# Kernel optimization log

Hardware: AMD Instinct MI355X
Metric: run time of the kernel (lower is better)

The kernel has to match this reference:

```python
import jax, jax.numpy as jnp
import numpy as np
import math

FACTOR = 5


def _prob_attention(queries, keys, values, index_sample):
    # queries/keys/values: [B, H, L, D]; index_sample: [L_Q, sample_k] int
    B, H, L_Q, D = queries.shape
    L_K = keys.shape[2]
    u = min(FACTOR * int(math.ceil(math.log(L_Q))), L_Q)  # n_top queries

    # --- _prob_QK: random-sampled scores, heuristic M, top-u query selection ---
    # gather sampled keys per query position: [B, H, L_Q, sample_k, D]
    K_sample = keys[:, :, index_sample, :]
    Q_K_sample = jnp.einsum('bhqd,bhqkd->bhqk', queries, K_sample)  # [B,H,L_Q,sample_k]
    M = Q_K_sample.max(axis=-1) - Q_K_sample.sum(axis=-1) / L_K      # [B,H,L_Q]
    M_top = jax.lax.top_k(M, u)[1]                                   # [B,H,u] indices

    # gather the selected queries and compute full scores against all keys
    Q_reduce = jnp.take_along_axis(queries, M_top[..., None], axis=2)  # [B,H,u,D]
    scores = jnp.einsum('bhud,bhkd->bhuk', Q_reduce, keys)             # [B,H,u,L_K]

    # scale: original does `scale = self.scale or 1/sqrt(D)`; with scale=True this
    # multiplies by True (i.e. *1), so scores are left unscaled -- faithful.

    # --- causal ProbMask: triu(1) rows gathered at the selected query indices ---
    causal = jnp.triu(jnp.ones((L_Q, L_K), dtype=bool), 1)  # [L_Q, L_K]
    row_mask = causal[M_top]                                 # [B,H,u,L_K]
    scores = jnp.where(row_mask, -jnp.inf, scores)

    attn = jax.nn.softmax(scores, axis=-1)                   # [B,H,u,L_K]

    # --- initial context (mask_flag=True): cumulative sum of V over time ---
    context = jnp.cumsum(values, axis=2)                     # [B,H,L_Q,D]

    # --- scatter-update context at selected query positions ---
    upd = jnp.einsum('bhuk,bhkd->bhud', attn, values)        # [B,H,u,D]
    b_idx = jnp.arange(B)[:, None, None]
    h_idx = jnp.arange(H)[None, :, None]
    context = context.at[b_idx, h_idx, M_top].set(upd)

    return jnp.transpose(context, (0, 2, 1, 3))              # [B,L_Q,H,D]


def setup_inputs() -> dict:
    key = jax.random.key(0)
    kq, kk, kv, ki = jax.random.split(key, 4)
    B, H, L, D = 4, 8, 2048, 64
    sample_k = FACTOR * int(math.ceil(math.log(L)))  # 40
    queries = jax.random.normal(kq, (B, H, L, D), dtype=jnp.float32)
    keys = jax.random.normal(kk, (B, H, L, D), dtype=jnp.float32)
    values = jax.random.normal(kv, (B, H, L, D), dtype=jnp.float32)
    index_sample = jax.random.randint(ki, (L, sample_k), 0, L)
    return {"queries": queries, "keys": keys, "values": values,
            "index_sample": index_sample}


def reference(queries, keys, values, index_sample):
    return _prob_attention(queries, keys, values, index_sample)
```

## Files before the change

### kernel.cpp

```cpp
#include <hip/hip_runtime.h>
#include <math.h>

#define B_ 4
#define H_ 8
#define L_ 2048
#define D_ 64
#define SK_ 40
#define U_ 40
#define NSEG 32
#define SEGLEN 64
#define CK 256
#define NCHUNK (L_ / CK)
#define QG 8
#define NQG (U_ / QG)

__global__ __launch_bounds__(1024) void k_compute_M(
    const float* __restrict__ Q, const float* __restrict__ K,
    const int* __restrict__ idxs, float* __restrict__ M) {
  int blk = blockIdx.x;
  int x = blk & 7;
  int j = blk >> 3;
  int bh = ((j >> 7) << 3) | x;
  int qc = j & 127;
  int wave = threadIdx.x >> 6;
  int lane = threadIdx.x & 63;
  int q = qc * 16 + wave;

  int g  = lane >> 3;
  int li = lane & 7;

  const float4* qrow = (const float4*)(Q + ((size_t)bh * L_ + q) * D_);
  float4 qa = qrow[li], qb = qrow[li + 8];
  int myidx = (lane < SK_) ? idxs[q * SK_ + lane] : 0;
  const float* Kb = K + (size_t)bh * L_ * D_;

  int kis[5];
#pragma unroll
  for (int t = 0; t < 5; ++t) kis[t] = __shfl(myidx, t * 8 + g, 64);
  float4 ka[5], kb[5];
#pragma unroll
  for (int t = 0; t < 5; ++t) {
    const float4* kr = (const float4*)(Kb + (size_t)kis[t] * D_);
    ka[t] = kr[li];
    kb[t] = kr[li + 8];
  }

  float d[5];
#pragma unroll
  for (int t = 0; t < 5; ++t) {
    d[t] = qa.x * ka[t].x + qa.y * ka[t].y + qa.z * ka[t].z + qa.w * ka[t].w
         + qb.x * kb[t].x + qb.y * kb[t].y + qb.z * kb[t].z + qb.w * kb[t].w;
  }
  float mx = -INFINITY, sm = 0.f;
#pragma unroll
  for (int t = 0; t < 5; ++t) {
    float v = d[t];
    v += __shfl_xor(v, 1, 64);
    v += __shfl_xor(v, 2, 64);
    v += __shfl_xor(v, 4, 64);
    mx = fmaxf(mx, v);
    sm += v;
  }
  mx = fmaxf(mx, __shfl_xor(mx, 8, 64));
  mx = fmaxf(mx, __shfl_xor(mx, 16, 64));
  mx = fmaxf(mx, __shfl_xor(mx, 32, 64));
  sm += __shfl_xor(sm, 8, 64);
  sm += __shfl_xor(sm, 16, 64);
  sm += __shfl_xor(sm, 32, 64);
  if (lane == 0) M[bh * L_ + q] = mx - sm * (1.0f / (float)L_);
}

__global__ __launch_bounds__(1024) void k_topk(
    const float* __restrict__ M, int* __restrict__ Mtop) {
  __shared__ unsigned keys[L_];
  __shared__ int hist[256];
  __shared__ int Gs[256];
  __shared__ unsigned ctl_prefix;
  __shared__ int ctl_need, ctl_cnt, ctl_min;
  __shared__ int wmin[16];
  int bh = blockIdx.x;
  int tid = threadIdx.x;

  for (int i = tid; i < L_; i += 1024) {
    unsigned u = __float_as_uint(M[bh * L_ + i]);
    keys[i] = (u & 0x80000000u) ? ~u : (u | 0x80000000u);
  }
  if (tid == 0) { ctl_prefix = 0u; ctl_need = U_; ctl_cnt = 0; }
  __syncthreads();

  unsigned prefix = 0u, pmask = 0u;
#pragma unroll
  for (int pass = 0; pass < 4; ++pass) {
    int shift = 24 - 8 * pass;
    if (tid < 256) hist[tid] = 0;
    __syncthreads();
    for (int i = tid; i < L_; i += 1024) {
      unsigned k = keys[i];
      if ((k & pmask) == prefix) atomicAdd(&hist[(k >> shift) & 0xffu], 1);
    }
    __syncthreads();
    if (tid < 64) {
      int b0 = tid * 4;
      int h0 = hist[b0], h1 = hist[b0 + 1], h2 = hist[b0 + 2], h3 = hist[b0 + 3];
      int gs = h0 + h1 + h2 + h3;
      int S = gs;
#pragma unroll
      for (int d = 1; d < 64; d <<= 1) {
        int v = __shfl_down(S, d, 64);
        if (tid + d < 64) S += v;
      }
      int E = S - gs;
      Gs[b0 + 3] = E;
      Gs[b0 + 2] = E + h3;
      Gs[b0 + 1] = E + h3 + h2;
      Gs[b0 + 0] = E + h3 + h2 + h1;
    }
    __syncthreads();
    int need = ctl_need;
    if (tid < 256) {
      int G = Gs[tid], h = hist[tid];
      if (G < need && need <= G + h) {
        ctl_prefix = prefix | ((unsigned)tid << shift);
        ctl_need = need - G;
      }
    }
    __syncthreads();
    prefix = ctl_prefix;
    pmask |= (0xffu << shift);
  }

  unsigned v40 = prefix;
  int tiesNeeded = ctl_need;
  __syncthreads();

  for (int i = tid; i < L_; i += 1024) {
    if (keys[i] > v40) {
      int slot = atomicAdd(&ctl_cnt, 1);
      Mtop[bh * U_ + slot] = i;
    }
  }
  __syncthreads();
  int base = ctl_cnt;
  int last = -1;
  for (int t = 0; t < tiesNeeded; ++t) {
    int lmin = 0x7fffffff;
    for (int i = tid; i < L_; i += 1024)
      if (keys[i] == v40 && i > last) lmin = min(lmin, i);
#pragma unroll
    for (int d = 32; d > 0; d >>= 1) lmin = min(lmin, __shfl_xor(lmin, d, 64));
    if ((tid & 63) == 0) wmin[tid >> 6] = lmin;
    __syncthreads();
    if (tid == 0) {
      int m = wmin[0];
      for (int w = 1; w < 16; ++w) m = min(m, wmin[w]);
      Mtop[bh * U_ + base + t] = m;
      ctl_min = m;
    }
    __syncthreads();
    last = ctl_min;
  }
}

__global__ __launch_bounds__(256) void k_segsum(
    const float* __restrict__ V, float* __restrict__ segsum) {
  int gw = (blockIdx.x * blockDim.x + threadIdx.x) >> 6;
  int lane = threadIdx.x & 63;
  int seg = gw & (NSEG - 1);
  int bh  = gw >> 5;
  const float* Vb = V + ((size_t)bh * L_ + seg * SEGLEN) * D_;
  float s = 0.f;
#pragma unroll 8
  for (int l = 0; l < SEGLEN; ++l) s += Vb[(size_t)l * D_ + lane];
  segsum[((size_t)bh * NSEG + seg) * D_ + lane] = s;
}

__global__ __launch_bounds__(256) void k_cumsum(
    const float* __restrict__ V, const float* __restrict__ segsum,
    float* __restrict__ out) {
  int gw = (blockIdx.x * blockDim.x + threadIdx.x) >> 6;
  int lane = threadIdx.x & 63;
  int seg = gw & (NSEG - 1);
  int bh  = gw >> 5;
  int b = bh >> 3, h = bh & 7;
  float off = 0.f;
  for (int s = 0; s < seg; ++s)
    off += segsum[((size_t)bh * NSEG + s) * D_ + lane];
  const float* Vb = V + ((size_t)bh * L_ + seg * SEGLEN) * D_;
  float run = off;
  for (int l = 0; l < SEGLEN; ++l) {
    run += Vb[(size_t)l * D_ + lane];
    int gl = seg * SEGLEN + l;
    out[(((size_t)b * L_ + gl) * H_ + h) * D_ + lane] = run;
  }
}

__global__ __launch_bounds__(256) void k_attn_part(
    const float* __restrict__ Q, const float* __restrict__ K,
    const float* __restrict__ V, const int* __restrict__ Mtop,
    float* __restrict__ pm, float* __restrict__ ps, float* __restrict__ pacc) {
  int blk = blockIdx.x;
  int x = blk & 7;
  int j = blk >> 3;
  int bh = (j / 40) * 8 + x;
  int rem = j % 40;
  int c  = rem / NQG;
  int qg = rem % NQG;

  int tid = threadIdx.x;
  int w = tid >> 6, lane = tid & 63;
  __shared__ float Qs[QG][D_];
  __shared__ float P[QG][CK];
  __shared__ float pvred[4][QG][D_];
  __shared__ int q0s[QG];
  if (tid < QG) q0s[tid] = Mtop[bh * U_ + qg * QG + tid];
  __syncthreads();
  for (int i = tid; i < QG * D_; i += 256) {
    int u = i >> 6, d = i & 63;
    Qs[u][d] = Q[((size_t)bh * L_ + q0s[u]) * D_ + d];
  }
  __syncthreads();

  int kg = c * CK + tid;
  const float4* kr = (const float4*)(K + ((size_t)bh * L_ + kg) * D_);
  float4 kv[16];
#pragma unroll
  for (int j4 = 0; j4 < 16; ++j4) kv[j4] = kr[j4];
#pragma unroll
  for (int u = 0; u < QG; ++u) {
    float acc = 0.f;
#pragma unroll
    for (int j4 = 0; j4 < 16; ++j4) {
      float4 qv = *(const float4*)&Qs[u][j4 * 4];
      acc += qv.x * kv[j4].x + qv.y * kv[j4].y + qv.z * kv[j4].z + qv.w * kv[j4].w;
    }
    P[u][tid] = (kg <= q0s[u]) ? acc : -INFINITY;
  }
  __syncthreads();

#pragma unroll
  for (int uu = 0; uu < 2; ++uu) {
    int u = w * 2 + uu;
    float v0 = P[u][lane], v1 = P[u][lane + 64];
    float v2 = P[u][lane + 128], v3 = P[u][lane + 192];
    float m = fmaxf(fmaxf(v0, v1), fmaxf(v2, v3));
    for (int o = 32; o > 0; o >>= 1) m = fmaxf(m, __shfl_xor(m, o, 64));
    float e0 = (v0 == -INFINITY) ? 0.f : expf(v0 - m);
    float e1 = (v1 == -INFINITY) ? 0.f : expf(v1 - m);
    float e2 = (v2 == -INFINITY) ? 0.f : expf(v2 - m);
    float e3 = (v3 == -INFINITY) ? 0.f : expf(v3 - m);
    float s = e0 + e1 + e2 + e3;
    for (int o = 32; o > 0; o >>= 1) s += __shfl_xor(s, o, 64);
    P[u][lane] = e0; P[u][lane + 64] = e1;
    P[u][lane + 128] = e2; P[u][lane + 192] = e3;
    if (lane == 0) {
      int p = (bh * NCHUNK + c) * U_ + qg * QG + u;
      pm[p] = m; ps[p] = s;
    }
  }
  __syncthreads();

  const float* Vb = V + ((size_t)bh * L_ + c * CK + w * 64) * D_;
  float acc[QG];
#pragma unroll
  for (int u = 0; u < QG; ++u) acc[u] = 0.f;
  for (int k4 = 0; k4 < 16; ++k4) {
    float4 pv[QG];
#pragma unroll
    for (int u = 0; u < QG; ++u) pv[u] = *(const float4*)&P[u][w * 64 + k4 * 4];
    float va = Vb[(size_t)(k4 * 4 + 0) * D_ + lane];
    float vb = Vb[(size_t)(k4 * 4 + 1) * D_ + lane];
    float vc = Vb[(size_t)(k4 * 4 + 2) * D_ + lane];
    float vd = Vb[(size_t)(k4 * 4 + 3) * D_ + lane];
#pragma unroll
    for (int u = 0; u < QG; ++u)
      acc[u] += pv[u].x * va + pv[u].y * vb + pv[u].z * vc + pv[u].w * vd;
  }
#pragma unroll
  for (int u = 0; u < QG; ++u) pvred[w][u][lane] = acc[u];
  __syncthreads();
#pragma unroll
  for (int uu = 0; uu < 2; ++uu) {
    int u = w * 2 + uu;
    float tot = pvred[0][u][lane] + pvred[1][u][lane] +
                pvred[2][u][lane] + pvred[3][u][lane];
    int p = (bh * NCHUNK + c) * U_ + qg * QG + u;
    pacc[(size_t)p * 64 + lane] = tot;
  }
}

__global__ __launch_bounds__(256) void k_attn_reduce(
    const float* __restrict__ pm, const float* __restrict__ ps,
    const float* __restrict__ pacc, const int* __restrict__ Mtop,
    float* __restrict__ out) {
  int g = blockIdx.x * 4 + (threadIdx.x >> 6);
  int lane = threadIdx.x & 63;
  int bh = g / U_, u = g % U_;
  int b = bh >> 3, h = bh & 7;
  int q0 = Mtop[bh * U_ + u];
  float pmv[NCHUNK];
  float M = -INFINITY;
#pragma unroll
  for (int c = 0; c < NCHUNK; ++c) {
    pmv[c] = pm[(bh * NCHUNK + c) * U_ + u];
    M = fmaxf(M, pmv[c]);
  }
  float T = 0.f, o = 0.f;
#pragma unroll
  for (int c = 0; c < NCHUNK; ++c) {
    float wgt = (pmv[c] == -INFINITY) ? 0.f : expf(pmv[c] - M);
    T += ps[(bh * NCHUNK + c) * U_ + u] * wgt;
    o += pacc[((size_t)(bh * NCHUNK + c) * U_ + u) * 64 + lane] * wgt;
  }
  out[(((size_t)b * L_ + q0) * H_ + h) * D_ + lane] = o / T;
}

extern "C" void kernel_launch(void* const* d_in, const int* in_sizes, int n_in,
                              void* d_out, int out_size, void* d_ws, size_t ws_size,
                              hipStream_t stream) {
  const float* Q = (const float*)d_in[0];
  const float* K = (const float*)d_in[1];
  const float* V = (const float*)d_in[2];
  const int* idxs = (const int*)d_in[3];
  float* out = (float*)d_out;

  char* ws = (char*)d_ws;
  float* M      = (float*)(ws + 0);
  float* segsum = (float*)(ws + 262144);
  int*   Mtop   = (int*)(ws + 524288);
  float* pm     = (float*)(ws + 532480);
  float* ps     = (float*)(ws + 573440);
  float* pacc   = (float*)(ws + 614400);

  k_compute_M<<<(B_ * H_ * L_) / 16, 1024, 0, stream>>>(Q, K, idxs, M);
  k_topk<<<B_ * H_, 1024, 0, stream>>>(M, Mtop);
  k_segsum<<<(B_ * H_ * NSEG) / 4, 256, 0, stream>>>(V, segsum);
  k_cumsum<<<(B_ * H_ * NSEG) / 4, 256, 0, stream>>>(V, segsum, out);
  k_attn_part<<<B_ * H_ * NCHUNK * NQG, 256, 0, stream>>>(Q, K, V, Mtop, pm, ps, pacc);
  k_attn_reduce<<<(B_ * H_ * U_) / 4, 256, 0, stream>>>(pm, ps, pacc, Mtop, out);
}
```

Before: 84.29 us.

## Fuse chunked attention and reduction into single kernel with online softmax

Replaces the split-K attention partial kernel and separate reduction kernel with one kernel where each block iterates over all key chunks, keeping running max/sum and rescaling accumulators (online softmax). This removes a launch and the workspace round-trip for partial max, sum and accumulators. In exchange the grid shrinks by the chunk count, so each block does serial work over the full key length with lower parallelism.

After: 142.9 us. 69.5% more time.

```diff
diff --git a/kernel.cpp b/kernel.cpp
--- a/kernel.cpp
+++ b/kernel.cpp
@@ -37,6 +37,7 @@
   int kis[5];
 #pragma unroll
   for (int t = 0; t < 5; ++t) kis[t] = __shfl(myidx, t * 8 + g, 64);
+
   float4 ka[5], kb[5];
 #pragma unroll
   for (int t = 0; t < 5; ++t) {
@@ -194,23 +195,25 @@
   }
 }
 
-__global__ __launch_bounds__(256) void k_attn_part(
+__global__ __launch_bounds__(256) void k_attn(
     const float* __restrict__ Q, const float* __restrict__ K,
     const float* __restrict__ V, const int* __restrict__ Mtop,
-    float* __restrict__ pm, float* __restrict__ ps, float* __restrict__ pacc) {
+    float* __restrict__ out) {
   int blk = blockIdx.x;
   int x = blk & 7;
   int j = blk >> 3;
-  int bh = (j / 40) * 8 + x;
-  int rem = j % 40;
-  int c  = rem / NQG;
-  int qg = rem % NQG;
+  int bh = (j / NQG) * 8 + x;
+  int qg = j % NQG;
+  int b = bh >> 3, h = bh & 7;
 
   int tid = threadIdx.x;
   int w = tid >> 6, lane = tid & 63;
   __shared__ float Qs[QG][D_];
   __shared__ float P[QG][CK];
   __shared__ float pvred[4][QG][D_];
+  __shared__ float scaleO[QG];
+  __shared__ float pfac[QG];
+  __shared__ float sfin[QG];
   __shared__ int q0s[QG];
   if (tid < QG) q0s[tid] = Mtop[bh * U_ + qg * QG + tid];
   __syncthreads();
@@ -218,100 +221,94 @@
     int u = i >> 6, d = i & 63;
     Qs[u][d] = Q[((size_t)bh * L_ + q0s[u]) * D_ + d];
   }
-  __syncthreads();
-
-  int kg = c * CK + tid;
-  const float4* kr = (const float4*)(K + ((size_t)bh * L_ + kg) * D_);
-  float4 kv[16];
-#pragma unroll
-  for (int j4 = 0; j4 < 16; ++j4) kv[j4] = kr[j4];
-#pragma unroll
-  for (int u = 0; u < QG; ++u) {
-    float acc = 0.f;
-#pragma unroll
-    for (int j4 = 0; j4 < 16; ++j4) {
-      float4 qv = *(const float4*)&Qs[u][j4 * 4];
-      acc += qv.x * kv[j4].x + qv.y * kv[j4].y + qv.z * kv[j4].z + qv.w * kv[j4].w;
-    }
-    P[u][tid] = (kg <= q0s[u]) ? acc : -INFINITY;
-  }
-  __syncthreads();
-
-#pragma unroll
-  for (int uu = 0; uu < 2; ++uu) {
-    int u = w * 2 + uu;
-    float v0 = P[u][lane], v1 = P[u][lane + 64];
-    float v2 = P[u][lane + 128], v3 = P[u][lane + 192];
-    float m = fmaxf(fmaxf(v0, v1), fmaxf(v2, v3));
-    for (int o = 32; o > 0; o >>= 1) m = fmaxf(m, __shfl_xor(m, o, 64));
-    float e0 = (v0 == -INFINITY) ? 0.f : expf(v0 - m);
-    float e1 = (v1 == -INFINITY) ? 0.f : expf(v1 - m);
-    float e2 = (v2 == -INFINITY) ? 0.f : expf(v2 - m);
-    float e3 = (v3 == -INFINITY) ? 0.f : expf(v3 - m);
-    float s = e0 + e1 + e2 + e3;
-    for (int o = 32; o > 0; o >>= 1) s += __shfl_xor(s, o, 64);
-    P[u][lane] = e0; P[u][lane + 64] = e1;
-    P[u][lane + 128] = e2; P[u][lane + 192] = e3;
-    if (lane == 0) {
-      int p = (bh * NCHUNK + c) * U_ + qg * QG + u;
-      pm[p] = m; ps[p] = s;
-    }
-  }
-  __syncthreads();
-
-  const float* Vb = V + ((size_t)bh * L_ + c * CK + w * 64) * D_;
+
+  float m_run[2] = {-INFINITY, -INFINITY};
+  float s_run[2] = {0.f, 0.f};
   float acc[QG];
 #pragma unroll
   for (int u = 0; u < QG; ++u) acc[u] = 0.f;
-  for (int k4 = 0; k4 < 16; ++k4) {
-    float4 pv[QG];
-#pragma unroll
-    for (int u = 0; u < QG; ++u) pv[u] = *(const float4*)&P[u][w * 64 + k4 * 4];
-    float va = Vb[(size_t)(k4 * 4 + 0) * D_ + lane];
-    float vb = Vb[(size_t)(k4 * 4 + 1) * D_ + lane];
-    float vc = Vb[(size_t)(k4 * 4 + 2) * D_ + lane];
-    float vd = Vb[(size_t)(k4 * 4 + 3) * D_ + lane];
+  __syncthreads();
+
+  for (int c = 0; c < NCHUNK; ++c) {
+    int kg = c * CK + tid;
+    const float4* kr = (const float4*)(K + ((size_t)bh * L_ + kg) * D_);
+    float4 kv[16];
+#pragma unroll
+    for (int j4 = 0; j4 < 16; ++j4) kv[j4] = kr[j4];
+#pragma unroll
+    for (int u = 0; u < QG; ++u) {
+      float a = 0.f;
+#pragma unroll
+      for (int j4 = 0; j4 < 16; ++j4) {
+        float4 qv = *(const float4*)&Qs[u][j4 * 4];
+        a += qv.x * kv[j4].x + qv.y * kv[j4].y + qv.z * kv[j4].z + qv.w * kv[j4].w;
+      }
+      P[u][tid] = (kg <= q0s[u]) ? a : -INFINITY;
+    }
+    __syncthreads();
+
+#pragma unroll
+    for (int uu = 0; uu < 2; ++uu) {
+      int u = w * 2 + uu;
+      float v0 = P[u][lane], v1 = P[u][lane + 64];
+      float v2 = P[u][lane + 128], v3 = P[u][lane + 192];
+      float m = fmaxf(fmaxf(v0, v1), fmaxf(v2, v3));
+      for (int o = 32; o > 0; o >>= 1) m = fmaxf(m, __shfl_xor(m, o, 64));
+      float e0 = (v0 == -INFINITY) ? 0.f : expf(v0 - m);
+      float e1 = (v1 == -INFINITY) ? 0.f : expf(v1 - m);
+      float e2 = (v2 == -INFINITY) ? 0.f : expf(v2 - m);
+      float e3 = (v3 == -INFINITY) ? 0.f : expf(v3 - m);
+      float s = e0 + e1 + e2 + e3;
+      for (int o = 32; o > 0; o >>= 1) s += __shfl_xor(s, o, 64);
+      P[u][lane] = e0; P[u][lane + 64] = e1;
+      P[u][lane + 128] = e2; P[u][lane + 192] = e3;
+      float so, pf;
+      if (m == -INFINITY) {
+        so = 1.f; pf = 0.f;
+      } else {
+        float mnew = fmaxf(m_run[uu], m);
+        so = (m_run[uu] == -INFINITY) ? 0.f : expf(m_run[uu] - mnew);
+        pf = expf(m - mnew);
+        m_run[uu] = mnew;
+      }
+      s_run[uu] = s_run[uu] * so + s * pf;
+      if (lane == 0) { scaleO[u] = so; pfac[u] = pf; }
+    }
+    __syncthreads();
+
+    const float* Vb = V + ((size_t)bh * L_ + c * CK + w * 64) * D_;
+    float pv[QG];
+#pragma unroll
+    for (int u = 0; u < QG; ++u) pv[u] = 0.f;
+    for (int k4 = 0; k4 < 16; ++k4) {
+      float4 pw[QG];
+#pragma unroll
+      for (int u = 0; u < QG; ++u) pw[u] = *(const float4*)&P[u][w * 64 + k4 * 4];
+      float va = Vb[(size_t)(k4 * 4 + 0) * D_ + lane];
+      float vb = Vb[(size_t)(k4 * 4 + 1) * D_ + lane];
+      float vc = Vb[(size_t)(k4 * 4 + 2) * D_ + lane];
+      float vd = Vb[(size_t)(k4 * 4 + 3) * D_ + lane];
+#pragma unroll
+      for (int u = 0; u < QG; ++u)
+        pv[u] += pw[u].x * va + pw[u].y * vb + pw[u].z * vc + pw[u].w * vd;
+    }
 #pragma unroll
     for (int u = 0; u < QG; ++u)
-      acc[u] += pv[u].x * va + pv[u].y * vb + pv[u].z * vc + pv[u].w * vd;
-  }
+      acc[u] = acc[u] * scaleO[u] + pv[u] * pfac[u];
+    __syncthreads();
+  }
+
 #pragma unroll
   for (int u = 0; u < QG; ++u) pvred[w][u][lane] = acc[u];
+  if (lane == 0) { sfin[w * 2] = s_run[0]; sfin[w * 2 + 1] = s_run[1]; }
   __syncthreads();
 #pragma unroll
   for (int uu = 0; uu < 2; ++uu) {
     int u = w * 2 + uu;
     float tot = pvred[0][u][lane] + pvred[1][u][lane] +
                 pvred[2][u][lane] + pvred[3][u][lane];
-    int p = (bh * NCHUNK + c) * U_ + qg * QG + u;
-    pacc[(size_t)p * 64 + lane] = tot;
-  }
-}
-
-__global__ __launch_bounds__(256) void k_attn_reduce(
-    const float* __restrict__ pm, const float* __restrict__ ps,
-    const float* __restrict__ pacc, const int* __restrict__ Mtop,
-    float* __restrict__ out) {
-  int g = blockIdx.x * 4 + (threadIdx.x >> 6);
-  int lane = threadIdx.x & 63;
-  int bh = g / U_, u = g % U_;
-  int b = bh >> 3, h = bh & 7;
-  int q0 = Mtop[bh * U_ + u];
-  float pmv[NCHUNK];
-  float M = -INFINITY;
-#pragma unroll
-  for (int c = 0; c < NCHUNK; ++c) {
-    pmv[c] = pm[(bh * NCHUNK + c) * U_ + u];
-    M = fmaxf(M, pmv[c]);
-  }
-  float T = 0.f, o = 0.f;
-#pragma unroll
-  for (int c = 0; c < NCHUNK; ++c) {
-    float wgt = (pmv[c] == -INFINITY) ? 0.f : expf(pmv[c] - M);
-    T += ps[(bh * NCHUNK + c) * U_ + u] * wgt;
-    o += pacc[((size_t)(bh * NCHUNK + c) * U_ + u) * 64 + lane] * wgt;
-  }
-  out[(((size_t)b * L_ + q0) * H_ + h) * D_ + lane] = o / T;
+    out[(((size_t)b * L_ + q0s[u]) * H_ + h) * D_ + lane] = tot / sfin[u];
+  }
 }
 
 extern "C" void kernel_launch(void* const* d_in, const int* in_sizes, int n_in,
@@ -327,14 +324,10 @@
   float* M      = (float*)(ws + 0);
   float* segsum = (float*)(ws + 262144);
   int*   Mtop   = (int*)(ws + 524288);
-  float* pm     = (float*)(ws + 532480);
-  float* ps     = (float*)(ws + 573440);
-  float* pacc   = (float*)(ws + 614400);
 
   k_compute_M<<<(B_ * H_ * L_) / 16, 1024, 0, stream>>>(Q, K, idxs, M);
   k_topk<<<B_ * H_, 1024, 0, stream>>>(M, Mtop);
   k_segsum<<<(B_ * H_ * NSEG) / 4, 256, 0, stream>>>(V, segsum);
   k_cumsum<<<(B_ * H_ * NSEG) / 4, 256, 0, stream>>>(V, segsum, out);
-  k_attn_part<<<B_ * H_ * NCHUNK * NQG, 256, 0, stream>>>(Q, K, V, Mtop, pm, ps, pacc);
-  k_attn_reduce<<<(B_ * H_ * U_) / 4, 256, 0, stream>>>(pm, ps, pacc, Mtop, out);
-}
+  k_attn<<<B_ * H_ * NQG, 256, 0, stream>>>(Q, K, V, Mtop, out);
+}
```

## Fuse cumsum of V into the M-computation kernel as extra blocks

Applied to the files above, without the earlier changes.

Replaces the separate segment-sum and cumulative-sum kernels with 32 extra 1024-thread blocks prepended to the M-computation launch. Each extra block handles one (b,h) pair, computing 16 segment totals in shared memory and then writing the prefix sums. This removes two kernel launches and the segsum workspace round-trip, letting the cumsum overlap with the sampled-QK work. The trade-off is that each cumsum block is long-running and serial (128 rows per thread, two passes over V), and may become a tail on the fused launch.

New measurement: 69.18 us. -17.9%, faster.

```diff
diff --git a/kernel.cpp b/kernel.cpp
--- a/kernel.cpp
+++ b/kernel.cpp
@@ -7,17 +7,39 @@
 #define D_ 64
 #define SK_ 40
 #define U_ 40
-#define NSEG 32
-#define SEGLEN 64
 #define CK 256
 #define NCHUNK (L_ / CK)
 #define QG 8
 #define NQG (U_ / QG)
-
-__global__ __launch_bounds__(1024) void k_compute_M(
+#define CSB 32
+
+__global__ __launch_bounds__(1024) void k_mcs(
     const float* __restrict__ Q, const float* __restrict__ K,
-    const int* __restrict__ idxs, float* __restrict__ M) {
-  int blk = blockIdx.x;
+    const int* __restrict__ idxs, const float* __restrict__ V,
+    float* __restrict__ M, float* __restrict__ out) {
+  if (blockIdx.x < CSB) {
+    __shared__ float segtot[16][64];
+    int bh = blockIdx.x;
+    int b = bh >> 3, h = bh & 7;
+    int t = threadIdx.x;
+    int seg = t >> 6, d = t & 63;
+    const float* Vb = V + (size_t)bh * L_ * D_;
+    int base = seg * 128;
+    float s = 0.f;
+    for (int l = 0; l < 128; ++l) s += Vb[(size_t)(base + l) * D_ + d];
+    segtot[seg][d] = s;
+    __syncthreads();
+    float run = 0.f;
+    for (int ss = 0; ss < seg; ++ss) run += segtot[ss][d];
+    for (int l = 0; l < 128; ++l) {
+      int gl = base + l;
+      run += Vb[(size_t)gl * D_ + d];
+      out[(((size_t)b * L_ + gl) * H_ + h) * D_ + d] = run;
+    }
+    return;
+  }
+
+  int blk = blockIdx.x - CSB;
   int x = blk & 7;
   int j = blk >> 3;
   int bh = ((j >> 7) << 3) | x;
@@ -37,6 +59,7 @@
   int kis[5];
 #pragma unroll
   for (int t = 0; t < 5; ++t) kis[t] = __shfl(myidx, t * 8 + g, 64);
+
   float4 ka[5], kb[5];
 #pragma unroll
   for (int t = 0; t < 5; ++t) {
@@ -158,39 +181,6 @@
     }
     __syncthreads();
     last = ctl_min;
-  }
-}
-
-__global__ __launch_bounds__(256) void k_segsum(
-    const float* __restrict__ V, float* __restrict__ segsum) {
-  int gw = (blockIdx.x * blockDim.x + threadIdx.x) >> 6;
-  int lane = threadIdx.x & 63;
-  int seg = gw & (NSEG - 1);
-  int bh  = gw >> 5;
-  const float* Vb = V + ((size_t)bh * L_ + seg * SEGLEN) * D_;
-  float s = 0.f;
-#pragma unroll 8
-  for (int l = 0; l < SEGLEN; ++l) s += Vb[(size_t)l * D_ + lane];
-  segsum[((size_t)bh * NSEG + seg) * D_ + lane] = s;
-}
-
-__global__ __launch_bounds__(256) void k_cumsum(
-    const float* __restrict__ V, const float* __restrict__ segsum,
-    float* __restrict__ out) {
-  int gw = (blockIdx.x * blockDim.x + threadIdx.x) >> 6;
-  int lane = threadIdx.x & 63;
-  int seg = gw & (NSEG - 1);
-  int bh  = gw >> 5;
-  int b = bh >> 3, h = bh & 7;
-  float off = 0.f;
-  for (int s = 0; s < seg; ++s)
-    off += segsum[((size_t)bh * NSEG + s) * D_ + lane];
-  const float* Vb = V + ((size_t)bh * L_ + seg * SEGLEN) * D_;
-  float run = off;
-  for (int l = 0; l < SEGLEN; ++l) {
-    run += Vb[(size_t)l * D_ + lane];
-    int gl = seg * SEGLEN + l;
-    out[(((size_t)b * L_ + gl) * H_ + h) * D_ + lane] = run;
   }
 }
 
@@ -325,16 +315,13 @@
 
   char* ws = (char*)d_ws;
   float* M      = (float*)(ws + 0);
-  float* segsum = (float*)(ws + 262144);
-  int*   Mtop   = (int*)(ws + 524288);
-  float* pm     = (float*)(ws + 532480);
-  float* ps     = (float*)(ws + 573440);
-  float* pacc   = (float*)(ws + 614400);
-
-  k_compute_M<<<(B_ * H_ * L_) / 16, 1024, 0, stream>>>(Q, K, idxs, M);
+  int*   Mtop   = (int*)(ws + 262144);
+  float* pm     = (float*)(ws + 270336);
+  float* ps     = (float*)(ws + 311296);
+  float* pacc   = (float*)(ws + 352256);
+
+  k_mcs<<<CSB + (B_ * H_ * L_) / 16, 1024, 0, stream>>>(Q, K, idxs, V, M, out);
   k_topk<<<B_ * H_, 1024, 0, stream>>>(M, Mtop);
-  k_segsum<<<(B_ * H_ * NSEG) / 4, 256, 0, stream>>>(V, segsum);
-  k_cumsum<<<(B_ * H_ * NSEG) / 4, 256, 0, stream>>>(V, segsum, out);
   k_attn_part<<<B_ * H_ * NCHUNK * NQG, 256, 0, stream>>>(Q, K, V, Mtop, pm, ps, pacc);
   k_attn_reduce<<<(B_ * H_ * U_) / 4, 256, 0, stream>>>(pm, ps, pacc, Mtop, out);
 }
```
